# Kernel optimization log

Measured on AMD Instinct MI355X. Metric: run time of the kernel, lower is better.

The kernel has to match this reference:

```python
import jax, jax.numpy as jnp
import numpy as np

B, S, D = 4, 2048, 512
E, K = 8, 2
MH = 4 * D      # resmlp mlp hidden
EH = 2 * D      # expert hidden
EPS = 1e-5


def setup_inputs() -> dict:
    key = jax.random.key(0)
    ks = jax.random.split(key, 16)
    s = 0.02
    return {
        "x": jax.random.normal(ks[0], (B, S, D), dtype=jnp.float32),
        "ln1_g": jnp.ones((D,), jnp.float32), "ln1_b": jnp.zeros((D,), jnp.float32),
        "w1": jax.random.normal(ks[1], (D, MH), jnp.float32) * s,
        "b1": jnp.zeros((MH,), jnp.float32),
        "w2": jax.random.normal(ks[2], (MH, D), jnp.float32) * s,
        "b2": jnp.zeros((D,), jnp.float32),
        "ln2_g": jnp.ones((D,), jnp.float32), "ln2_b": jnp.zeros((D,), jnp.float32),
        "wr": jax.random.normal(ks[3], (E, D), jnp.float32) * s,
        "ew1": jax.random.normal(ks[4], (E, D, EH), jnp.float32) * s,
        "eb1": jnp.zeros((E, EH), jnp.float32),
        "ew2": jax.random.normal(ks[5], (E, EH, D), jnp.float32) * s,
        "eb2": jnp.zeros((E, D), jnp.float32),
        "lnf_g": jnp.ones((D,), jnp.float32), "lnf_b": jnp.zeros((D,), jnp.float32),
    }


def _ln(z, g, b):
    m = z.mean(-1, keepdims=True)
    v = ((z - m) ** 2).mean(-1, keepdims=True)
    return (z - m) * jax.lax.rsqrt(v + EPS) * g + b


def reference(x, ln1_g, ln1_b, w1, b1, w2, b2, ln2_g, ln2_b,
              wr, ew1, eb1, ew2, eb2, lnf_g, lnf_b):
    # ---- ResidualMLPBlock (eval mode: dropout is identity) ----
    h = _ln(x, ln1_g, ln1_b)
    h = jax.nn.gelu(h @ w1 + b1, approximate=False) @ w2 + b2
    x = x + h
    x = _ln(x, ln2_g, ln2_b) + x
    # ---- MoE (eval: no jitter noise, aux_loss = 0) ----
    xf = x.reshape(-1, D)              # [N, D], N = B*S
    n = xf.shape[0]
    probs = jax.nn.softmax(xf @ wr.T, axis=-1)          # [N, E]
    topv, topi = jax.lax.top_k(probs, K)                # [N, K]
    topv = topv / topv.sum(-1, keepdims=True)
    # dense per-token gate per expert: sum over k of renormalized prob where idx==j
    gates = jnp.zeros((n, E), xf.dtype).at[jnp.arange(n)[:, None], topi].add(topv)
    # per-expert MLP over all tokens (masked scatter-combine via gates)
    he = jax.nn.gelu(jnp.einsum("nd,edh->enh", xf, ew1) + eb1[:, None, :],
                     approximate=False)                 # [E, N, 2D]
    ye = jnp.einsum("enh,ehd->end", he, ew2) + eb2[:, None, :]  # [E, N, D]
    out = jnp.einsum("ne,end->nd", gates, ye).reshape(B, S, D)
    # ---- final LayerNorm ----
    out = _ln(out, lnf_g, lnf_b)
    aux_loss = jnp.zeros((), x.dtype)  # eval mode
    return out, aux_loss
```

## Files before the change

kernel.cpp:

```cpp
#include <hip/hip_runtime.h>

#define NTOK 8192
#define DIM  512
#define MHID 2048
#define EHID 1024
#define NEXP 8
#define RBLK 64

using half_t = _Float16;
typedef _Float16 f16x8 __attribute__((ext_vector_type(8)));
typedef float    f32x4 __attribute__((ext_vector_type(4)));

__device__ __forceinline__ float gelu_exact(float v) {
    return 0.5f * v * (1.0f + erff(v * 0.70710678118654752f));
}

__device__ __forceinline__ f16x8 f16x8_zero() {
    f16x8 v;
#pragma unroll
    for (int i = 0; i < 8; i++) v[i] = (_Float16)0.f;
    return v;
}

__device__ __forceinline__ float block_sum4(float v, float* red, int tid) {
#pragma unroll
    for (int off = 32; off; off >>= 1) v += __shfl_down(v, off);
    if ((tid & 63) == 0) red[tid >> 6] = v;
    __syncthreads();
    float r = red[0] + red[1] + red[2] + red[3];
    __syncthreads();
    return r;
}

__global__ __launch_bounds__(256) void ln1_split_kernel(
    const float* __restrict__ x, const float* __restrict__ g, const float* __restrict__ b,
    half_t* __restrict__ xh, half_t* __restrict__ xl)
{
    const int row = blockIdx.x, tid = threadIdx.x;
    __shared__ float red[4];
    const size_t base = (size_t)row * DIM;
    float2 v = reinterpret_cast<const float2*>(x + base)[tid];
    float mean = block_sum4(v.x + v.y, red, tid) * (1.0f / DIM);
    float d0 = v.x - mean, d1 = v.y - mean;
    float var = block_sum4(d0 * d0 + d1 * d1, red, tid) * (1.0f / DIM);
    float rstd = rsqrtf(var + 1e-5f);
    int d = tid * 2;
    float y0 = d0 * rstd * g[d]     + b[d];
    float y1 = d1 * rstd * g[d + 1] + b[d + 1];
    half_t h0 = (half_t)y0, h1 = (half_t)y1;
    xh[base + d] = h0;  xh[base + d + 1] = h1;
    xl[base + d]     = (half_t)(y0 - (float)h0);
    xl[base + d + 1] = (half_t)(y1 - (float)h1);
}

__global__ __launch_bounds__(256) void resid_ln2_kernel(
    const float* __restrict__ x, float* __restrict__ hio,
    const float* __restrict__ g, const float* __restrict__ b,
    half_t* __restrict__ x3h)
{
    const int row = blockIdx.x, tid = threadIdx.x;
    __shared__ float red[4];
    const size_t base = (size_t)row * DIM;
    float2 xv = reinterpret_cast<const float2*>(x + base)[tid];
    float2 hv = reinterpret_cast<float2*>(hio + base)[tid];
    float z0 = xv.x + hv.x, z1 = xv.y + hv.y;
    float mean = block_sum4(z0 + z1, red, tid) * (1.0f / DIM);
    float d0 = z0 - mean, d1 = z1 - mean;
    float var = block_sum4(d0 * d0 + d1 * d1, red, tid) * (1.0f / DIM);
    float rstd = rsqrtf(var + 1e-5f);
    int d = tid * 2;
    float y0 = d0 * rstd * g[d]     + b[d]     + z0;
    float y1 = d1 * rstd * g[d + 1] + b[d + 1] + z1;
    float2 o; o.x = y0; o.y = y1;
    reinterpret_cast<float2*>(hio + base)[tid] = o;
    x3h[base + d]     = (half_t)y0;
    x3h[base + d + 1] = (half_t)y1;
}

__global__ void transpose_split_kernel(const float* __restrict__ in,
                                       half_t* __restrict__ oh, half_t* __restrict__ ol,
                                       int R, int C)
{
    __shared__ float t[32][33];
    const size_t mo = (size_t)blockIdx.z * (size_t)R * (size_t)C;
    const int c0 = blockIdx.x * 32, r0 = blockIdx.y * 32;
    const int tx = threadIdx.x, ty = threadIdx.y;
    for (int i = ty; i < 32; i += 8) t[i][tx] = in[mo + (size_t)(r0 + i) * C + c0 + tx];
    __syncthreads();
    for (int i = ty; i < 32; i += 8) {
        float v = t[tx][i];
        size_t o = mo + (size_t)(c0 + i) * R + r0 + tx;
        half_t h = (half_t)v;
        oh[o] = h;
        if (ol) ol[o] = (half_t)(v - (float)h);
    }
}

template <int EPI>
__global__ __launch_bounds__(256) void gemm3_kernel(
    const half_t* __restrict__ A0, const half_t* __restrict__ A1,
    const half_t* __restrict__ B0, const half_t* __restrict__ B1,
    const float* __restrict__ bias,
    float* __restrict__ Cf, half_t* __restrict__ Ch, half_t* __restrict__ Cl,
    int M, int Nc, int K)
{
    __shared__ half_t As[2][128][40];
    __shared__ half_t Bs[2][128][40];
    const int m0 = blockIdx.x * 128, n0 = blockIdx.y * 128;
    const int tid = threadIdx.x;
    const int lane = tid & 63, wid = tid >> 6;
    const int wr = wid >> 1, wc = wid & 1;
    f32x4 acc[4][4];
#pragma unroll
    for (int i = 0; i < 4; i++)
#pragma unroll
        for (int j = 0; j < 4; j++)
#pragma unroll
            for (int q = 0; q < 4; q++) acc[i][j][q] = 0.f;

    const int sm = tid >> 1, sk = (tid & 1) * 16;
    const size_t aoff = (size_t)(m0 + sm) * K + sk;
    const size_t boff = (size_t)(n0 + sm) * K + sk;
    const int kk = (lane >> 4) * 8;
    const int fr = lane & 15;

#pragma unroll 1
    for (int k0 = 0; k0 < K; k0 += 32) {
        __syncthreads();
        *(f16x8*)&As[0][sm][sk]     = *(const f16x8*)(A0 + aoff + k0);
        *(f16x8*)&As[0][sm][sk + 8] = *(const f16x8*)(A0 + aoff + k0 + 8);
        *(f16x8*)&As[1][sm][sk]     = *(const f16x8*)(A1 + aoff + k0);
        *(f16x8*)&As[1][sm][sk + 8] = *(const f16x8*)(A1 + aoff + k0 + 8);
        *(f16x8*)&Bs[0][sm][sk]     = *(const f16x8*)(B0 + boff + k0);
        *(f16x8*)&Bs[0][sm][sk + 8] = *(const f16x8*)(B0 + boff + k0 + 8);
        *(f16x8*)&Bs[1][sm][sk]     = *(const f16x8*)(B1 + boff + k0);
        *(f16x8*)&Bs[1][sm][sk + 8] = *(const f16x8*)(B1 + boff + k0 + 8);
        __syncthreads();
        f16x8 ah[4], al[4], bh[4], bl[4];
#pragma unroll
        for (int i = 0; i < 4; i++) {
            ah[i] = *(const f16x8*)&As[0][wr * 64 + i * 16 + fr][kk];
            al[i] = *(const f16x8*)&As[1][wr * 64 + i * 16 + fr][kk];
            bh[i] = *(const f16x8*)&Bs[0][wc * 64 + i * 16 + fr][kk];
            bl[i] = *(const f16x8*)&Bs[1][wc * 64 + i * 16 + fr][kk];
        }
#pragma unroll
        for (int i = 0; i < 4; i++)
#pragma unroll
            for (int j = 0; j < 4; j++) {
                acc[i][j] = __builtin_amdgcn_mfma_f32_16x16x32_f16(ah[i], bh[j], acc[i][j], 0, 0, 0);
                acc[i][j] = __builtin_amdgcn_mfma_f32_16x16x32_f16(al[i], bh[j], acc[i][j], 0, 0, 0);
                acc[i][j] = __builtin_amdgcn_mfma_f32_16x16x32_f16(ah[i], bl[j], acc[i][j], 0, 0, 0);
            }
    }

    const int rl = (lane >> 4) * 4, cl = lane & 15;
#pragma unroll
    for (int i = 0; i < 4; i++) {
#pragma unroll
        for (int j = 0; j < 4; j++) {
            int cc = n0 + wc * 64 + j * 16 + cl;
            float bv = bias[cc];
#pragma unroll
            for (int q = 0; q < 4; q++) {
                int rr = m0 + wr * 64 + i * 16 + rl + q;
                float v = acc[i][j][q] + bv;
                size_t o = (size_t)rr * Nc + cc;
                if (EPI == 1) {
                    float ge = gelu_exact(v);
                    half_t h = (half_t)ge;
                    Ch[o] = h;
                    Cl[o] = (half_t)(ge - (float)h);
                } else {
                    Cf[o] = v;
                }
            }
        }
    }
}

__global__ __launch_bounds__(256) void router_kernel(
    const float* __restrict__ x3, const float* __restrict__ wrm,
    int* __restrict__ cnt, int* __restrict__ aid, float* __restrict__ gate)
{
    __shared__ float wl[NEXP][DIM];
    __shared__ int   texp[RBLK * 2];
    __shared__ float tgate[RBLK * 2];
    __shared__ int   lslot[RBLK * 2];
    __shared__ int   lcnt[NEXP], lbase[NEXP];
    const int tid = threadIdx.x;
    for (int i = tid; i < NEXP * DIM / 4; i += 256)
        reinterpret_cast<float4*>(&wl[0][0])[i] = reinterpret_cast<const float4*>(wrm)[i];
    if (tid < NEXP) lcnt[tid] = 0;
    __syncthreads();
    const int w = tid >> 6, lane = tid & 63;
#pragma unroll 1
    for (int t = 0; t < RBLK / 4; ++t) {
        const int lt = w * (RBLK / 4) + t;
        const int token = blockIdx.x * RBLK + lt;
        const float* xr = x3 + (size_t)token * DIM;
        float a[NEXP];
#pragma unroll
        for (int e = 0; e < NEXP; e++) a[e] = 0.f;
#pragma unroll
        for (int d0 = 0; d0 < DIM; d0 += 64) {
            float xv = xr[d0 + lane];
#pragma unroll
            for (int e = 0; e < NEXP; e++) a[e] += xv * wl[e][d0 + lane];
        }
#pragma unroll
        for (int e = 0; e < NEXP; e++)
#pragma unroll
            for (int off = 32; off; off >>= 1) a[e] += __shfl_xor(a[e], off);
        if (lane == 0) {
            int i1 = 0; float v1 = a[0];
#pragma unroll
            for (int e = 1; e < NEXP; e++) if (a[e] > v1) { v1 = a[e]; i1 = e; }
            int i2 = -1; float v2 = -3.4e38f;
#pragma unroll
            for (int e = 0; e < NEXP; e++) if (e != i1 && a[e] > v2) { v2 = a[e]; i2 = e; }
            float e2 = expf(v2 - v1);
            float g1 = 1.0f / (1.0f + e2);
            texp[lt * 2]      = i1; tgate[lt * 2]      = g1;
            texp[lt * 2 + 1]  = i2; tgate[lt * 2 + 1]  = 1.0f - g1;
        }
    }
    __syncthreads();
    if (tid < RBLK * 2) lslot[tid] = atomicAdd(&lcnt[texp[tid]], 1);
    __syncthreads();
    if (tid < NEXP) lbase[tid] = atomicAdd(&cnt[tid * 32], lcnt[tid]);
    __syncthreads();
    if (tid < RBLK * 2) {
        const int e = texp[tid];
        const int asg = blockIdx.x * (RBLK * 2) + tid;
        aid[e * NTOK + lbase[e] + lslot[tid]] = asg;
        gate[asg] = tgate[tid];
    }
}

__global__ __launch_bounds__(256) void egemm1_kernel(
    const half_t* __restrict__ X,
    const half_t* __restrict__ W,
    const float* __restrict__ eb1,
    const int* __restrict__ cnt, const int* __restrict__ aid,
    half_t* __restrict__ He)
{
    const int bid = blockIdx.x;
    const int e = bid >> 9, rem = bid & 511;
    const int mt = rem >> 3, nt = rem & 7;
    const int ne = cnt[e * 32];
    if (mt * 128 >= ne) return;
    __shared__ half_t As[128][40];
    __shared__ half_t Bs[128][40];
    __shared__ int rowmap[128];
    const int tid = threadIdx.x;
    if (tid < 128) {
        int slot = mt * 128 + tid;
        rowmap[tid] = (slot < ne) ? aid[e * NTOK + slot] : -1;
    }
    __syncthreads();
    const int lane = tid & 63, wid = tid >> 6;
    const int wr = wid >> 1, wc = wid & 1;
    const int sm = tid >> 1, sk = (tid & 1) * 16;
    const int arow = rowmap[sm];
    const half_t* Ap = (arow >= 0) ? X + (size_t)(arow >> 1) * DIM + sk : (const half_t*)0;
    const half_t* Bp = W + (size_t)e * EHID * DIM + (size_t)(nt * 128 + sm) * DIM + sk;
    f32x4 acc[4][4];
#pragma unroll
    for (int i = 0; i < 4; i++)
#pragma unroll
        for (int j = 0; j < 4; j++)
#pragma unroll
            for (int q = 0; q < 4; q++) acc[i][j][q] = 0.f;
    const int kk = (lane >> 4) * 8, fr = lane & 15;
    const f16x8 zz = f16x8_zero();
#pragma unroll 1
    for (int k0 = 0; k0 < DIM; k0 += 32) {
        __syncthreads();
        if (Ap) {
            *(f16x8*)&As[sm][sk]     = *(const f16x8*)(Ap + k0);
            *(f16x8*)&As[sm][sk + 8] = *(const f16x8*)(Ap + k0 + 8);
        } else {
            *(f16x8*)&As[sm][sk]     = zz;
            *(f16x8*)&As[sm][sk + 8] = zz;
        }
        *(f16x8*)&Bs[sm][sk]     = *(const f16x8*)(Bp + k0);
        *(f16x8*)&Bs[sm][sk + 8] = *(const f16x8*)(Bp + k0 + 8);
        __syncthreads();
        f16x8 af[4], bf[4];
#pragma unroll
        for (int i = 0; i < 4; i++) af[i] = *(const f16x8*)&As[wr * 64 + i * 16 + fr][kk];
#pragma unroll
        for (int i = 0; i < 4; i++) bf[i] = *(const f16x8*)&Bs[wc * 64 + i * 16 + fr][kk];
#pragma unroll
        for (int i = 0; i < 4; i++)
#pragma unroll
            for (int j = 0; j < 4; j++)
                acc[i][j] = __builtin_amdgcn_mfma_f32_16x16x32_f16(af[i], bf[j], acc[i][j], 0, 0, 0);
    }
    const int rl = (lane >> 4) * 4, cl = lane & 15;
#pragma unroll
    for (int i = 0; i < 4; i++)
#pragma unroll
        for (int q = 0; q < 4; q++) {
            int r = wr * 64 + i * 16 + rl + q;
            int a = rowmap[r];
            if (a >= 0) {
#pragma unroll
                for (int j = 0; j < 4; j++) {
                    int cc = nt * 128 + wc * 64 + j * 16 + cl;
                    float v = acc[i][j][q] + eb1[e * EHID + cc];
                    He[(size_t)a * EHID + cc] = (half_t)gelu_exact(v);
                }
            }
        }
}

__global__ __launch_bounds__(256) void egemm2_kernel(
    const half_t* __restrict__ Hin,
    const half_t* __restrict__ W,
    const float* __restrict__ eb2,
    const int* __restrict__ cnt, const int* __restrict__ aid,
    const float* __restrict__ gate,
    float* __restrict__ Ye)
{
    const int bid = blockIdx.x;
    const int e = bid >> 8, rem = bid & 255;
    const int mt = rem >> 2, nt = rem & 3;
    const int ne = cnt[e * 32];
    if (mt * 128 >= ne) return;
    __shared__ half_t As[128][40];
    __shared__ half_t Bs[128][40];
    __shared__ int rowmap[128];
    const int tid = threadIdx.x;
    if (tid < 128) {
        int slot = mt * 128 + tid;
        rowmap[tid] = (slot < ne) ? aid[e * NTOK + slot] : -1;
    }
    __syncthreads();
    const int lane = tid & 63, wid = tid >> 6;
    const int wr = wid >> 1, wc = wid & 1;
    const int sm = tid >> 1, sk = (tid & 1) * 16;
    const int arow = rowmap[sm];
    const half_t* Ap = (arow >= 0) ? Hin + (size_t)arow * EHID + sk : (const half_t*)0;
    const half_t* Bp = W + (size_t)e * DIM * EHID + (size_t)(nt * 128 + sm) * EHID + sk;
    f32x4 acc[4][4];
#pragma unroll
    for (int i = 0; i < 4; i++)
#pragma unroll
        for (int j = 0; j < 4; j++)
#pragma unroll
            for (int q = 0; q < 4; q++) acc[i][j][q] = 0.f;
    const int kk = (lane >> 4) * 8, fr = lane & 15;
    const f16x8 zz = f16x8_zero();
#pragma unroll 1
    for (int k0 = 0; k0 < EHID; k0 += 32) {
        __syncthreads();
        if (Ap) {
            *(f16x8*)&As[sm][sk]     = *(const f16x8*)(Ap + k0);
            *(f16x8*)&As[sm][sk + 8] = *(const f16x8*)(Ap + k0 + 8);
        } else {
            *(f16x8*)&As[sm][sk]     = zz;
            *(f16x8*)&As[sm][sk + 8] = zz;
        }
        *(f16x8*)&Bs[sm][sk]     = *(const f16x8*)(Bp + k0);
        *(f16x8*)&Bs[sm][sk + 8] = *(const f16x8*)(Bp + k0 + 8);
        __syncthreads();
        f16x8 af[4], bf[4];
#pragma unroll
        for (int i = 0; i < 4; i++) af[i] = *(const f16x8*)&As[wr * 64 + i * 16 + fr][kk];
#pragma unroll
        for (int i = 0; i < 4; i++) bf[i] = *(const f16x8*)&Bs[wc * 64 + i * 16 + fr][kk];
#pragma unroll
        for (int i = 0; i < 4; i++)
#pragma unroll
            for (int j = 0; j < 4; j++)
                acc[i][j] = __builtin_amdgcn_mfma_f32_16x16x32_f16(af[i], bf[j], acc[i][j], 0, 0, 0);
    }
    const int rl = (lane >> 4) * 4, cl = lane & 15;
#pragma unroll
    for (int i = 0; i < 4; i++)
#pragma unroll
        for (int q = 0; q < 4; q++) {
            int r = wr * 64 + i * 16 + rl + q;
            int a = rowmap[r];
            if (a >= 0) {
                float gv = gate[a];
#pragma unroll
                for (int j = 0; j < 4; j++) {
                    int cc = nt * 128 + wc * 64 + j * 16 + cl;
                    float v = (acc[i][j][q] + eb2[e * DIM + cc]) * gv;
                    Ye[(size_t)a * DIM + cc] = v;
                }
            }
        }
}

__global__ __launch_bounds__(256) void combine_lnf_kernel(
    const float* __restrict__ Ye, const float* __restrict__ g, const float* __restrict__ b,
    float* __restrict__ out)
{
    const int t = blockIdx.x, tid = threadIdx.x;
    __shared__ float red[4];
    float2 y0 = reinterpret_cast<const float2*>(Ye + (size_t)(2 * t) * DIM)[tid];
    float2 y1 = reinterpret_cast<const float2*>(Ye + (size_t)(2 * t + 1) * DIM)[tid];
    float z0 = y0.x + y1.x, z1 = y0.y + y1.y;
    float mean = block_sum4(z0 + z1, red, tid) * (1.0f / DIM);
    float d0 = z0 - mean, d1 = z1 - mean;
    float var = block_sum4(d0 * d0 + d1 * d1, red, tid) * (1.0f / DIM);
    float rstd = rsqrtf(var + 1e-5f);
    int d = tid * 2;
    out[(size_t)t * DIM + d]     = d0 * rstd * g[d]     + b[d];
    out[(size_t)t * DIM + d + 1] = d1 * rstd * g[d + 1] + b[d + 1];
    if (t == 0 && tid == 0) out[(size_t)NTOK * DIM] = 0.f;
}

__global__ void zero_cnt_kernel(int* cnt) {
    cnt[threadIdx.x] = 0;
}

extern "C" void kernel_launch(void* const* d_in, const int* in_sizes, int n_in,
                              void* d_out, int out_size, void* d_ws, size_t ws_size,
                              hipStream_t stream)
{
    (void)in_sizes; (void)n_in; (void)out_size; (void)ws_size;
    const float* x    = (const float*)d_in[0];
    const float* ln1g = (const float*)d_in[1];
    const float* ln1b = (const float*)d_in[2];
    const float* w1   = (const float*)d_in[3];
    const float* b1   = (const float*)d_in[4];
    const float* w2   = (const float*)d_in[5];
    const float* b2   = (const float*)d_in[6];
    const float* ln2g = (const float*)d_in[7];
    const float* ln2b = (const float*)d_in[8];
    const float* wrm  = (const float*)d_in[9];
    const float* ew1  = (const float*)d_in[10];
    const float* eb1  = (const float*)d_in[11];
    const float* ew2  = (const float*)d_in[12];
    const float* eb2  = (const float*)d_in[13];
    const float* lnfg = (const float*)d_in[14];
    const float* lnfb = (const float*)d_in[15];
    float* out = (float*)d_out;

    char* w = (char*)d_ws;
    size_t off = 0;
    auto take = [&](size_t bytes) {
        char* p = w + off;
        off += bytes;
        off = (off + 255) & ~(size_t)255;
        return p;
    };
    half_t* xh_h  = (half_t*)take((size_t)NTOK * DIM * 2);
    half_t* xh_l  = (half_t*)take((size_t)NTOK * DIM * 2);
    half_t* w1t_h = (half_t*)take((size_t)DIM * MHID * 2);
    half_t* w1t_l = (half_t*)take((size_t)DIM * MHID * 2);
    half_t* w2t_h = (half_t*)take((size_t)MHID * DIM * 2);
    half_t* w2t_l = (half_t*)take((size_t)MHID * DIM * 2);
    char*   big   = take((size_t)NTOK * MHID * 2 * 2);
    half_t* a1h   = (half_t*)big;
    half_t* a1l   = (half_t*)(big + (size_t)NTOK * MHID * 2);
    half_t* heh   = (half_t*)big;
    float*  yef   = (float*)(big + (size_t)NTOK * MHID * 2);
    float*  x3f   = (float*)take((size_t)NTOK * DIM * 4);
    half_t* x3h   = (half_t*)take((size_t)NTOK * DIM * 2);
    half_t* ew1t  = (half_t*)take((size_t)NEXP * DIM * EHID * 2);
    half_t* ew2t  = (half_t*)take((size_t)NEXP * EHID * DIM * 2);
    int*    cnt   = (int*)take(1024);
    int*    aid   = (int*)take((size_t)NEXP * NTOK * 4);
    float*  gate  = (float*)take((size_t)NTOK * 2 * 4);

    zero_cnt_kernel<<<1, 256, 0, stream>>>(cnt);
    ln1_split_kernel<<<NTOK, 256, 0, stream>>>(x, ln1g, ln1b, xh_h, xh_l);
    transpose_split_kernel<<<dim3(MHID / 32, DIM / 32, 1), dim3(32, 8), 0, stream>>>(w1, w1t_h, w1t_l, DIM, MHID);
    transpose_split_kernel<<<dim3(DIM / 32, MHID / 32, 1), dim3(32, 8), 0, stream>>>(w2, w2t_h, w2t_l, MHID, DIM);
    transpose_split_kernel<<<dim3(EHID / 32, DIM / 32, NEXP), dim3(32, 8), 0, stream>>>(ew1, ew1t, (half_t*)0, DIM, EHID);
    transpose_split_kernel<<<dim3(DIM / 32, EHID / 32, NEXP), dim3(32, 8), 0, stream>>>(ew2, ew2t, (half_t*)0, EHID, DIM);
    gemm3_kernel<1><<<dim3(NTOK / 128, MHID / 128), 256, 0, stream>>>(
        xh_h, xh_l, w1t_h, w1t_l, b1, (float*)0, a1h, a1l, NTOK, MHID, DIM);
    gemm3_kernel<0><<<dim3(NTOK / 128, DIM / 128), 256, 0, stream>>>(
        a1h, a1l, w2t_h, w2t_l, b2, x3f, (half_t*)0, (half_t*)0, NTOK, DIM, MHID);
    resid_ln2_kernel<<<NTOK, 256, 0, stream>>>(x, x3f, ln2g, ln2b, x3h);
    router_kernel<<<NTOK / RBLK, 256, 0, stream>>>(x3f, wrm, cnt, aid, gate);
    egemm1_kernel<<<NEXP * (NTOK / 128) * (EHID / 128), 256, 0, stream>>>(x3h, ew1t, eb1, cnt, aid, heh);
    egemm2_kernel<<<NEXP * (NTOK / 128) * (DIM / 128), 256, 0, stream>>>(heh, ew2t, eb2, cnt, aid, gate, yef);
    combine_lnf_kernel<<<NTOK, 256, 0, stream>>>(yef, lnfg, lnfb, out);
}
```

Measured before the change: 349.3 us.

## Switch GEMMs to 32x32 MFMA with direct-to-LDS loads, swizzle, split-K

All GEMM kernels move from 16x16x32 to 32x32x16 MFMA tiles and stage tiles with global_load_lds directly into an XOR-swizzled unpadded LDS layout. The second dense GEMM is split along K into two halves, writing partial sums to separate buffers. The residual/LN2 kernel sums those partials and adds b2. The aim is fewer LDS instructions, fewer bank conflicts and more blocks for the narrow N=512 GEMM, at the cost of an extra partial-sum buffer pass. Invalid expert rows now load row 0 instead of zeros, which is harmless because the epilogue masks them. The second partial reuses the xh_h buffer, which is no longer needed by then.

Result: faster. 324.4 us (-7.1%).

```diff
diff --git a/kernel.cpp b/kernel.cpp
--- a/kernel.cpp
+++ b/kernel.cpp
@@ -9,17 +9,18 @@
 
 using half_t = _Float16;
 typedef _Float16 f16x8 __attribute__((ext_vector_type(8)));
-typedef float    f32x4 __attribute__((ext_vector_type(4)));
+typedef float    f32x16 __attribute__((ext_vector_type(16)));
+
+#define MFMA32(a, b, c) __builtin_amdgcn_mfma_f32_32x32x16_f16((a), (b), (c), 0, 0, 0)
+
+typedef const __attribute__((address_space(1))) void* gas_ptr;
+typedef __attribute__((address_space(3))) void*       las_ptr;
+__device__ __forceinline__ void gl16(const void* g, void* l) {
+    __builtin_amdgcn_global_load_lds((gas_ptr)g, (las_ptr)l, 16, 0, 0);
+}
 
 __device__ __forceinline__ float gelu_exact(float v) {
     return 0.5f * v * (1.0f + erff(v * 0.70710678118654752f));
-}
-
-__device__ __forceinline__ f16x8 f16x8_zero() {
-    f16x8 v;
-#pragma unroll
-    for (int i = 0; i < 8; i++) v[i] = (_Float16)0.f;
-    return v;
 }
 
 __device__ __forceinline__ float block_sum4(float v, float* red, int tid) {
@@ -54,7 +55,8 @@
 }
 
 __global__ __launch_bounds__(256) void resid_ln2_kernel(
-    const float* __restrict__ x, float* __restrict__ hio,
+    const float* __restrict__ x, float* __restrict__ p0, const float* __restrict__ p1,
+    const float* __restrict__ b2,
     const float* __restrict__ g, const float* __restrict__ b,
     half_t* __restrict__ x3h)
 {
@@ -62,8 +64,10 @@
     __shared__ float red[4];
     const size_t base = (size_t)row * DIM;
     float2 xv = reinterpret_cast<const float2*>(x + base)[tid];
-    float2 hv = reinterpret_cast<float2*>(hio + base)[tid];
-    float z0 = xv.x + hv.x, z1 = xv.y + hv.y;
+    float2 h0 = reinterpret_cast<float2*>(p0 + base)[tid];
+    float2 h1 = reinterpret_cast<const float2*>(p1 + base)[tid];
+    float2 bb = reinterpret_cast<const float2*>(b2)[tid];
+    float z0 = xv.x + h0.x + h1.x + bb.x, z1 = xv.y + h0.y + h1.y + bb.y;
     float mean = block_sum4(z0 + z1, red, tid) * (1.0f / DIM);
     float d0 = z0 - mean, d1 = z1 - mean;
     float var = block_sum4(d0 * d0 + d1 * d1, red, tid) * (1.0f / DIM);
@@ -72,7 +76,7 @@
     float y0 = d0 * rstd * g[d]     + b[d]     + z0;
     float y1 = d1 * rstd * g[d + 1] + b[d + 1] + z1;
     float2 o; o.x = y0; o.y = y1;
-    reinterpret_cast<float2*>(hio + base)[tid] = o;
+    reinterpret_cast<float2*>(p0 + base)[tid] = o;
     x3h[base + d]     = (half_t)y0;
     x3h[base + d + 1] = (half_t)y1;
 }
@@ -101,70 +105,97 @@
     const half_t* __restrict__ A0, const half_t* __restrict__ A1,
     const half_t* __restrict__ B0, const half_t* __restrict__ B1,
     const float* __restrict__ bias,
-    float* __restrict__ Cf, half_t* __restrict__ Ch, half_t* __restrict__ Cl,
-    int M, int Nc, int K)
-{
-    __shared__ half_t As[2][128][40];
-    __shared__ half_t Bs[2][128][40];
+    float* __restrict__ Cf0, float* __restrict__ Cf1,
+    half_t* __restrict__ Ch, half_t* __restrict__ Cl,
+    int Nc, int K, int Ktile)
+{
+    __shared__ __align__(16) half_t As0[128 * 32];
+    __shared__ __align__(16) half_t As1[128 * 32];
+    __shared__ __align__(16) half_t Bs0[128 * 32];
+    __shared__ __align__(16) half_t Bs1[128 * 32];
     const int m0 = blockIdx.x * 128, n0 = blockIdx.y * 128;
+    const int kbeg = blockIdx.z * Ktile;
+    float* Cf = blockIdx.z ? Cf1 : Cf0;
     const int tid = threadIdx.x;
     const int lane = tid & 63, wid = tid >> 6;
     const int wr = wid >> 1, wc = wid & 1;
-    f32x4 acc[4][4];
-#pragma unroll
-    for (int i = 0; i < 4; i++)
-#pragma unroll
-        for (int j = 0; j < 4; j++)
-#pragma unroll
-            for (int q = 0; q < 4; q++) acc[i][j][q] = 0.f;
-
-    const int sm = tid >> 1, sk = (tid & 1) * 16;
-    const size_t aoff = (size_t)(m0 + sm) * K + sk;
-    const size_t boff = (size_t)(n0 + sm) * K + sk;
-    const int kk = (lane >> 4) * 8;
-    const int fr = lane & 15;
+
+    const int c0 = tid, c1 = tid + 256;
+    const int r0 = c0 >> 2, s0 = (c0 & 3) ^ ((r0 >> 1) & 3);
+    const int r1 = c1 >> 2, s1 = (c1 & 3) ^ ((r1 >> 1) & 3);
+    const size_t aoff0 = (size_t)(m0 + r0) * K + kbeg + s0 * 8;
+    const size_t aoff1 = (size_t)(m0 + r1) * K + kbeg + s1 * 8;
+    const size_t boff0 = (size_t)(n0 + r0) * K + kbeg + s0 * 8;
+    const size_t boff1 = (size_t)(n0 + r1) * K + kbeg + s1 * 8;
+
+    const int l31 = lane & 31, l5 = lane >> 5;
+    int oa[2][2], ob[2][2];
+#pragma unroll
+    for (int i = 0; i < 2; i++)
+#pragma unroll
+        for (int kh = 0; kh < 2; kh++) {
+            int ra = wr * 64 + i * 32 + l31;
+            oa[i][kh] = ra * 32 + (((l5 + kh * 2) ^ ((ra >> 1) & 3)) << 3);
+            int rb = wc * 64 + i * 32 + l31;
+            ob[i][kh] = rb * 32 + (((l5 + kh * 2) ^ ((rb >> 1) & 3)) << 3);
+        }
+
+    f32x16 acc[2][2];
+#pragma unroll
+    for (int i = 0; i < 2; i++)
+#pragma unroll
+        for (int j = 0; j < 2; j++)
+#pragma unroll
+            for (int q = 0; q < 16; q++) acc[i][j][q] = 0.f;
 
 #pragma unroll 1
-    for (int k0 = 0; k0 < K; k0 += 32) {
+    for (int k0 = 0; k0 < Ktile; k0 += 32) {
         __syncthreads();
-        *(f16x8*)&As[0][sm][sk]     = *(const f16x8*)(A0 + aoff + k0);
-        *(f16x8*)&As[0][sm][sk + 8] = *(const f16x8*)(A0 + aoff + k0 + 8);
-        *(f16x8*)&As[1][sm][sk]     = *(const f16x8*)(A1 + aoff + k0);
-        *(f16x8*)&As[1][sm][sk + 8] = *(const f16x8*)(A1 + aoff + k0 + 8);
-        *(f16x8*)&Bs[0][sm][sk]     = *(const f16x8*)(B0 + boff + k0);
-        *(f16x8*)&Bs[0][sm][sk + 8] = *(const f16x8*)(B0 + boff + k0 + 8);
-        *(f16x8*)&Bs[1][sm][sk]     = *(const f16x8*)(B1 + boff + k0);
-        *(f16x8*)&Bs[1][sm][sk + 8] = *(const f16x8*)(B1 + boff + k0 + 8);
+        gl16(A0 + aoff0 + k0, As0 + c0 * 8);
+        gl16(A0 + aoff1 + k0, As0 + c1 * 8);
+        gl16(A1 + aoff0 + k0, As1 + c0 * 8);
+        gl16(A1 + aoff1 + k0, As1 + c1 * 8);
+        gl16(B0 + boff0 + k0, Bs0 + c0 * 8);
+        gl16(B0 + boff1 + k0, Bs0 + c1 * 8);
+        gl16(B1 + boff0 + k0, Bs1 + c0 * 8);
+        gl16(B1 + boff1 + k0, Bs1 + c1 * 8);
         __syncthreads();
-        f16x8 ah[4], al[4], bh[4], bl[4];
-#pragma unroll
-        for (int i = 0; i < 4; i++) {
-            ah[i] = *(const f16x8*)&As[0][wr * 64 + i * 16 + fr][kk];
-            al[i] = *(const f16x8*)&As[1][wr * 64 + i * 16 + fr][kk];
-            bh[i] = *(const f16x8*)&Bs[0][wc * 64 + i * 16 + fr][kk];
-            bl[i] = *(const f16x8*)&Bs[1][wc * 64 + i * 16 + fr][kk];
-        }
-#pragma unroll
-        for (int i = 0; i < 4; i++)
-#pragma unroll
-            for (int j = 0; j < 4; j++) {
-                acc[i][j] = __builtin_amdgcn_mfma_f32_16x16x32_f16(ah[i], bh[j], acc[i][j], 0, 0, 0);
-                acc[i][j] = __builtin_amdgcn_mfma_f32_16x16x32_f16(al[i], bh[j], acc[i][j], 0, 0, 0);
-                acc[i][j] = __builtin_amdgcn_mfma_f32_16x16x32_f16(ah[i], bl[j], acc[i][j], 0, 0, 0);
-            }
-    }
-
-    const int rl = (lane >> 4) * 4, cl = lane & 15;
-#pragma unroll
-    for (int i = 0; i < 4; i++) {
-#pragma unroll
-        for (int j = 0; j < 4; j++) {
-            int cc = n0 + wc * 64 + j * 16 + cl;
-            float bv = bias[cc];
-#pragma unroll
-            for (int q = 0; q < 4; q++) {
-                int rr = m0 + wr * 64 + i * 16 + rl + q;
-                float v = acc[i][j][q] + bv;
+#pragma unroll
+        for (int kh = 0; kh < 2; kh++) {
+            f16x8 ah0 = *(const f16x8*)(As0 + oa[0][kh]);
+            f16x8 ah1 = *(const f16x8*)(As0 + oa[1][kh]);
+            f16x8 al0 = *(const f16x8*)(As1 + oa[0][kh]);
+            f16x8 al1 = *(const f16x8*)(As1 + oa[1][kh]);
+            f16x8 bh0 = *(const f16x8*)(Bs0 + ob[0][kh]);
+            f16x8 bh1 = *(const f16x8*)(Bs0 + ob[1][kh]);
+            f16x8 bl0 = *(const f16x8*)(Bs1 + ob[0][kh]);
+            f16x8 bl1 = *(const f16x8*)(Bs1 + ob[1][kh]);
+            acc[0][0] = MFMA32(ah0, bh0, acc[0][0]);
+            acc[0][0] = MFMA32(al0, bh0, acc[0][0]);
+            acc[0][0] = MFMA32(ah0, bl0, acc[0][0]);
+            acc[0][1] = MFMA32(ah0, bh1, acc[0][1]);
+            acc[0][1] = MFMA32(al0, bh1, acc[0][1]);
+            acc[0][1] = MFMA32(ah0, bl1, acc[0][1]);
+            acc[1][0] = MFMA32(ah1, bh0, acc[1][0]);
+            acc[1][0] = MFMA32(al1, bh0, acc[1][0]);
+            acc[1][0] = MFMA32(ah1, bl0, acc[1][0]);
+            acc[1][1] = MFMA32(ah1, bh1, acc[1][1]);
+            acc[1][1] = MFMA32(al1, bh1, acc[1][1]);
+            acc[1][1] = MFMA32(ah1, bl1, acc[1][1]);
+        }
+    }
+
+    const int er = 4 * l5;
+#pragma unroll
+    for (int i = 0; i < 2; i++)
+#pragma unroll
+        for (int j = 0; j < 2; j++) {
+            int cc = n0 + wc * 64 + j * 32 + l31;
+            float bv = (EPI == 1) ? bias[cc] : 0.f;
+#pragma unroll
+            for (int reg = 0; reg < 16; reg++) {
+                int rr = m0 + wr * 64 + i * 32 + er + 8 * (reg >> 2) + (reg & 3);
+                float v = acc[i][j][reg] + bv;
                 size_t o = (size_t)rr * Nc + cc;
                 if (EPI == 1) {
                     float ge = gelu_exact(v);
@@ -176,7 +207,6 @@
                 }
             }
         }
-    }
 }
 
 __global__ __launch_bounds__(256) void router_kernel(
@@ -250,8 +280,8 @@
     const int mt = rem >> 3, nt = rem & 7;
     const int ne = cnt[e * 32];
     if (mt * 128 >= ne) return;
-    __shared__ half_t As[128][40];
-    __shared__ half_t Bs[128][40];
+    __shared__ __align__(16) half_t As[128 * 32];
+    __shared__ __align__(16) half_t Bs[128 * 32];
     __shared__ int rowmap[128];
     const int tid = threadIdx.x;
     if (tid < 128) {
@@ -261,55 +291,66 @@
     __syncthreads();
     const int lane = tid & 63, wid = tid >> 6;
     const int wr = wid >> 1, wc = wid & 1;
-    const int sm = tid >> 1, sk = (tid & 1) * 16;
-    const int arow = rowmap[sm];
-    const half_t* Ap = (arow >= 0) ? X + (size_t)(arow >> 1) * DIM + sk : (const half_t*)0;
-    const half_t* Bp = W + (size_t)e * EHID * DIM + (size_t)(nt * 128 + sm) * DIM + sk;
-    f32x4 acc[4][4];
-#pragma unroll
-    for (int i = 0; i < 4; i++)
-#pragma unroll
-        for (int j = 0; j < 4; j++)
-#pragma unroll
-            for (int q = 0; q < 4; q++) acc[i][j][q] = 0.f;
-    const int kk = (lane >> 4) * 8, fr = lane & 15;
-    const f16x8 zz = f16x8_zero();
+    const int c0 = tid, c1 = tid + 256;
+    const int r0 = c0 >> 2, s0 = (c0 & 3) ^ ((r0 >> 1) & 3);
+    const int r1 = c1 >> 2, s1 = (c1 & 3) ^ ((r1 >> 1) & 3);
+    const int a0r = rowmap[r0], a1r = rowmap[r1];
+    const half_t* pa0 = X + (size_t)(a0r >= 0 ? (a0r >> 1) : 0) * DIM + s0 * 8;
+    const half_t* pa1 = X + (size_t)(a1r >= 0 ? (a1r >> 1) : 0) * DIM + s1 * 8;
+    const half_t* pb0 = W + (size_t)e * EHID * DIM + (size_t)(nt * 128 + r0) * DIM + s0 * 8;
+    const half_t* pb1 = W + (size_t)e * EHID * DIM + (size_t)(nt * 128 + r1) * DIM + s1 * 8;
+
+    const int l31 = lane & 31, l5 = lane >> 5;
+    int oa[2][2], ob[2][2];
+#pragma unroll
+    for (int i = 0; i < 2; i++)
+#pragma unroll
+        for (int kh = 0; kh < 2; kh++) {
+            int ra = wr * 64 + i * 32 + l31;
+            oa[i][kh] = ra * 32 + (((l5 + kh * 2) ^ ((ra >> 1) & 3)) << 3);
+            int rb = wc * 64 + i * 32 + l31;
+            ob[i][kh] = rb * 32 + (((l5 + kh * 2) ^ ((rb >> 1) & 3)) << 3);
+        }
+    f32x16 acc[2][2];
+#pragma unroll
+    for (int i = 0; i < 2; i++)
+#pragma unroll
+        for (int j = 0; j < 2; j++)
+#pragma unroll
+            for (int q = 0; q < 16; q++) acc[i][j][q] = 0.f;
+
 #pragma unroll 1
     for (int k0 = 0; k0 < DIM; k0 += 32) {
         __syncthreads();
-        if (Ap) {
-            *(f16x8*)&As[sm][sk]     = *(const f16x8*)(Ap + k0);
-            *(f16x8*)&As[sm][sk + 8] = *(const f16x8*)(Ap + k0 + 8);
-        } else {
-            *(f16x8*)&As[sm][sk]     = zz;
-            *(f16x8*)&As[sm][sk + 8] = zz;
-        }
-        *(f16x8*)&Bs[sm][sk]     = *(const f16x8*)(Bp + k0);
-        *(f16x8*)&Bs[sm][sk + 8] = *(const f16x8*)(Bp + k0 + 8);
+        gl16(pa0 + k0, As + c0 * 8);
+        gl16(pa1 + k0, As + c1 * 8);
+        gl16(pb0 + k0, Bs + c0 * 8);
+        gl16(pb1 + k0, Bs + c1 * 8);
         __syncthreads();
-        f16x8 af[4], bf[4];
-#pragma unroll
-        for (int i = 0; i < 4; i++) af[i] = *(const f16x8*)&As[wr * 64 + i * 16 + fr][kk];
-#pragma unroll
-        for (int i = 0; i < 4; i++) bf[i] = *(const f16x8*)&Bs[wc * 64 + i * 16 + fr][kk];
-#pragma unroll
-        for (int i = 0; i < 4; i++)
-#pragma unroll
-            for (int j = 0; j < 4; j++)
-                acc[i][j] = __builtin_amdgcn_mfma_f32_16x16x32_f16(af[i], bf[j], acc[i][j], 0, 0, 0);
-    }
-    const int rl = (lane >> 4) * 4, cl = lane & 15;
-#pragma unroll
-    for (int i = 0; i < 4; i++)
-#pragma unroll
-        for (int q = 0; q < 4; q++) {
-            int r = wr * 64 + i * 16 + rl + q;
-            int a = rowmap[r];
+#pragma unroll
+        for (int kh = 0; kh < 2; kh++) {
+            f16x8 a0 = *(const f16x8*)(As + oa[0][kh]);
+            f16x8 a1 = *(const f16x8*)(As + oa[1][kh]);
+            f16x8 b0 = *(const f16x8*)(Bs + ob[0][kh]);
+            f16x8 b1 = *(const f16x8*)(Bs + ob[1][kh]);
+            acc[0][0] = MFMA32(a0, b0, acc[0][0]);
+            acc[0][1] = MFMA32(a0, b1, acc[0][1]);
+            acc[1][0] = MFMA32(a1, b0, acc[1][0]);
+            acc[1][1] = MFMA32(a1, b1, acc[1][1]);
+        }
+    }
+    const int er = 4 * l5;
+#pragma unroll
+    for (int i = 0; i < 2; i++)
+#pragma unroll
+        for (int reg = 0; reg < 16; reg++) {
+            int rloc = wr * 64 + i * 32 + er + 8 * (reg >> 2) + (reg & 3);
+            int a = rowmap[rloc];
             if (a >= 0) {
 #pragma unroll
-                for (int j = 0; j < 4; j++) {
-                    int cc = nt * 128 + wc * 64 + j * 16 + cl;
-                    float v = acc[i][j][q] + eb1[e * EHID + cc];
+                for (int j = 0; j < 2; j++) {
+                    int cc = nt * 128 + wc * 64 + j * 32 + l31;
+                    float v = acc[i][j][reg] + eb1[e * EHID + cc];
                     He[(size_t)a * EHID + cc] = (half_t)gelu_exact(v);
                 }
             }
@@ -329,8 +370,8 @@
     const int mt = rem >> 2, nt = rem & 3;
     const int ne = cnt[e * 32];
     if (mt * 128 >= ne) return;
-    __shared__ half_t As[128][40];
-    __shared__ half_t Bs[128][40];
+    __shared__ __align__(16) half_t As[128 * 32];
+    __shared__ __align__(16) half_t Bs[128 * 32];
     __shared__ int rowmap[128];
     const int tid = threadIdx.x;
     if (tid < 128) {
@@ -340,56 +381,67 @@
     __syncthreads();
     const int lane = tid & 63, wid = tid >> 6;
     const int wr = wid >> 1, wc = wid & 1;
-    const int sm = tid >> 1, sk = (tid & 1) * 16;
-    const int arow = rowmap[sm];
-    const half_t* Ap = (arow >= 0) ? Hin + (size_t)arow * EHID + sk : (const half_t*)0;
-    const half_t* Bp = W + (size_t)e * DIM * EHID + (size_t)(nt * 128 + sm) * EHID + sk;
-    f32x4 acc[4][4];
-#pragma unroll
-    for (int i = 0; i < 4; i++)
-#pragma unroll
-        for (int j = 0; j < 4; j++)
-#pragma unroll
-            for (int q = 0; q < 4; q++) acc[i][j][q] = 0.f;
-    const int kk = (lane >> 4) * 8, fr = lane & 15;
-    const f16x8 zz = f16x8_zero();
+    const int c0 = tid, c1 = tid + 256;
+    const int r0 = c0 >> 2, s0 = (c0 & 3) ^ ((r0 >> 1) & 3);
+    const int r1 = c1 >> 2, s1 = (c1 & 3) ^ ((r1 >> 1) & 3);
+    const int a0r = rowmap[r0], a1r = rowmap[r1];
+    const half_t* pa0 = Hin + (size_t)(a0r >= 0 ? a0r : 0) * EHID + s0 * 8;
+    const half_t* pa1 = Hin + (size_t)(a1r >= 0 ? a1r : 0) * EHID + s1 * 8;
+    const half_t* pb0 = W + (size_t)e * DIM * EHID + (size_t)(nt * 128 + r0) * EHID + s0 * 8;
+    const half_t* pb1 = W + (size_t)e * DIM * EHID + (size_t)(nt * 128 + r1) * EHID + s1 * 8;
+
+    const int l31 = lane & 31, l5 = lane >> 5;
+    int oa[2][2], ob[2][2];
+#pragma unroll
+    for (int i = 0; i < 2; i++)
+#pragma unroll
+        for (int kh = 0; kh < 2; kh++) {
+            int ra = wr * 64 + i * 32 + l31;
+            oa[i][kh] = ra * 32 + (((l5 + kh * 2) ^ ((ra >> 1) & 3)) << 3);
+            int rb = wc * 64 + i * 32 + l31;
+            ob[i][kh] = rb * 32 + (((l5 + kh * 2) ^ ((rb >> 1) & 3)) << 3);
+        }
+    f32x16 acc[2][2];
+#pragma unroll
+    for (int i = 0; i < 2; i++)
+#pragma unroll
+        for (int j = 0; j < 2; j++)
+#pragma unroll
+            for (int q = 0; q < 16; q++) acc[i][j][q] = 0.f;
+
 #pragma unroll 1
     for (int k0 = 0; k0 < EHID; k0 += 32) {
         __syncthreads();
-        if (Ap) {
-            *(f16x8*)&As[sm][sk]     = *(const f16x8*)(Ap + k0);
-            *(f16x8*)&As[sm][sk + 8] = *(const f16x8*)(Ap + k0 + 8);
-        } else {
-            *(f16x8*)&As[sm][sk]     = zz;
-            *(f16x8*)&As[sm][sk + 8] = zz;
-        }
-        *(f16x8*)&Bs[sm][sk]     = *(const f16x8*)(Bp + k0);
-        *(f16x8*)&Bs[sm][sk + 8] = *(const f16x8*)(Bp + k0 + 8);
+        gl16(pa0 + k0, As + c0 * 8);
+        gl16(pa1 + k0, As + c1 * 8);
+        gl16(pb0 + k0, Bs + c0 * 8);
+        gl16(pb1 + k0, Bs + c1 * 8);
         __syncthreads();
-        f16x8 af[4], bf[4];
-#pragma unroll
-        for (int i = 0; i < 4; i++) af[i] = *(const f16x8*)&As[wr * 64 + i * 16 + fr][kk];
-#pragma unroll
-        for (int i = 0; i < 4; i++) bf[i] = *(const f16x8*)&Bs[wc * 64 + i * 16 + fr][kk];
-#pragma unroll
-        for (int i = 0; i < 4; i++)
-#pragma unroll
-            for (int j = 0; j < 4; j++)
-                acc[i][j] = __builtin_amdgcn_mfma_f32_16x16x32_f16(af[i], bf[j], acc[i][j], 0, 0, 0);
-    }
-    const int rl = (lane >> 4) * 4, cl = lane & 15;
-#pragma unroll
-    for (int i = 0; i < 4; i++)
-#pragma unroll
-        for (int q = 0; q < 4; q++) {
-            int r = wr * 64 + i * 16 + rl + q;
-            int a = rowmap[r];
+#pragma unroll
+        for (int kh = 0; kh < 2; kh++) {
+            f16x8 a0 = *(const f16x8*)(As + oa[0][kh]);
+            f16x8 a1 = *(const f16x8*)(As + oa[1][kh]);
+            f16x8 b0 = *(const f16x8*)(Bs + ob[0][kh]);
+            f16x8 b1 = *(const f16x8*)(Bs + ob[1][kh]);
+            acc[0][0] = MFMA32(a0, b0, acc[0][0]);
+            acc[0][1] = MFMA32(a0, b1, acc[0][1]);
+            acc[1][0] = MFMA32(a1, b0, acc[1][0]);
+            acc[1][1] = MFMA32(a1, b1, acc[1][1]);
+        }
+    }
+    const int er = 4 * l5;
+#pragma unroll
+    for (int i = 0; i < 2; i++)
+#pragma unroll
+        for (int reg = 0; reg < 16; reg++) {
+            int rloc = wr * 64 + i * 32 + er + 8 * (reg >> 2) + (reg & 3);
+            int a = rowmap[rloc];
             if (a >= 0) {
                 float gv = gate[a];
 #pragma unroll
-                for (int j = 0; j < 4; j++) {
-                    int cc = nt * 128 + wc * 64 + j * 16 + cl;
-                    float v = (acc[i][j][q] + eb2[e * DIM + cc]) * gv;
+                for (int j = 0; j < 2; j++) {
+                    int cc = nt * 128 + wc * 64 + j * 32 + l31;
+                    float v = (acc[i][j][reg] + eb2[e * DIM + cc]) * gv;
                     Ye[(size_t)a * DIM + cc] = v;
                 }
             }
@@ -469,17 +521,20 @@
     int*    aid   = (int*)take((size_t)NEXP * NTOK * 4);
     float*  gate  = (float*)take((size_t)NTOK * 2 * 4);
 
+    float* p0 = x3f;
+    float* p1 = (float*)xh_h;
+
     zero_cnt_kernel<<<1, 256, 0, stream>>>(cnt);
     ln1_split_kernel<<<NTOK, 256, 0, stream>>>(x, ln1g, ln1b, xh_h, xh_l);
     transpose_split_kernel<<<dim3(MHID / 32, DIM / 32, 1), dim3(32, 8), 0, stream>>>(w1, w1t_h, w1t_l, DIM, MHID);
     transpose_split_kernel<<<dim3(DIM / 32, MHID / 32, 1), dim3(32, 8), 0, stream>>>(w2, w2t_h, w2t_l, MHID, DIM);
     transpose_split_kernel<<<dim3(EHID / 32, DIM / 32, NEXP), dim3(32, 8), 0, stream>>>(ew1, ew1t, (half_t*)0, DIM, EHID);
     transpose_split_kernel<<<dim3(DIM / 32, EHID / 32, NEXP), dim3(32, 8), 0, stream>>>(ew2, ew2t, (half_t*)0, EHID, DIM);
-    gemm3_kernel<1><<<dim3(NTOK / 128, MHID / 128), 256, 0, stream>>>(
-        xh_h, xh_l, w1t_h, w1t_l, b1, (float*)0, a1h, a1l, NTOK, MHID, DIM);
-    gemm3_kernel<0><<<dim3(NTOK / 128, DIM / 128), 256, 0, stream>>>(
-        a1h, a1l, w2t_h, w2t_l, b2, x3f, (half_t*)0, (half_t*)0, NTOK, DIM, MHID);
-    resid_ln2_kernel<<<NTOK, 256, 0, stream>>>(x, x3f, ln2g, ln2b, x3h);
+    gemm3_kernel<1><<<dim3(NTOK / 128, MHID / 128, 1), 256, 0, stream>>>(
+        xh_h, xh_l, w1t_h, w1t_l, b1, (float*)0, (float*)0, a1h, a1l, MHID, DIM, DIM);
+    gemm3_kernel<0><<<dim3(NTOK / 128, DIM / 128, 2), 256, 0, stream>>>(
+        a1h, a1l, w2t_h, w2t_l, (const float*)0, p0, p1, (half_t*)0, (half_t*)0, DIM, MHID, MHID / 2);
+    resid_ln2_kernel<<<NTOK, 256, 0, stream>>>(x, p0, p1, b2, ln2g, ln2b, x3h);
     router_kernel<<<NTOK / RBLK, 256, 0, stream>>>(x3f, wrm, cnt, aid, gate);
     egemm1_kernel<<<NEXP * (NTOK / 128) * (EHID / 128), 256, 0, stream>>>(x3h, ew1t, eb1, cnt, aid, heh);
     egemm2_kernel<<<NEXP * (NTOK / 128) * (DIM / 128), 256, 0, stream>>>(heh, ew2t, eb2, cnt, aid, gate, yef);
```
